# Kernel optimization log

Measured on AMD Instinct MI355X. Metric: run time of the kernel, lower is better.

The kernel has to match this reference:

```python
import jax, jax.numpy as jnp
import numpy as np
from jax import lax

IN_CH, OUT_CH, K = 64, 64, 3
FAN_IN = 8           # LogicNets-style fan-in per output channel (over C_in*K taps)
IN_SCALE, IN_BITS = 0.0625, 8
OUT_SCALE, OUT_BITS = 0.125, 8


def make_mask(seed=7):
    # Binary mask [OUT_CH, IN_CH, K] with exactly FAN_IN ones per output channel
    rng = np.random.RandomState(seed)
    m = np.zeros((OUT_CH, IN_CH * K), dtype=np.float32)
    for o in range(OUT_CH):
        idx = rng.choice(IN_CH * K, size=FAN_IN, replace=False)
        m[o, idx] = 1.0
    return jnp.asarray(m.reshape(OUT_CH, IN_CH, K))


def fake_quant(v, scale, bits):
    # symmetric fake quantization with straight-through estimator
    qmin = -(2 ** (bits - 1))
    qmax = 2 ** (bits - 1) - 1
    q = jnp.clip(jnp.round(v / scale), qmin, qmax) * scale
    return v + lax.stop_gradient(q - v)


def setup_inputs() -> dict:
    key = jax.random.key(0)
    k1, k2 = jax.random.split(key)
    x = jax.random.normal(k1, (512, IN_CH, 1024), dtype=jnp.float32)
    weight = jax.random.normal(k2, (OUT_CH, IN_CH, K), dtype=jnp.float32) * 0.1
    mask = make_mask()
    return {"x": x, "weight": weight, "mask": mask}


def reference(x, weight, mask):
    # input quant
    xq = fake_quant(x, IN_SCALE, IN_BITS)
    # masked (sparse) conv1d, padding=1 (same length)
    w = weight * mask
    out = lax.conv_general_dilated(
        xq, w,
        window_strides=(1,),
        padding=[(1, 1)],
        dimension_numbers=("NCH", "OIH", "NCH"),
    )
    # output quant
    return fake_quant(out, OUT_SCALE, OUT_BITS)
```

## Files before the change

### kernel.cpp

```cpp
#include <hip/hip_runtime.h>

namespace {
constexpr int kInCh  = 64;
constexpr int kOutCh = 64;
constexpr int kK     = 3;
constexpr int kFanIn = 8;
constexpr int kH     = 1024;
constexpr int kTile  = 128;
constexpr int kRow   = kTile + 8;
constexpr int kBlk   = 512;
}

struct Tap { int off; float w; };

__device__ __forceinline__ float quant_in(float v) {
    float q = rintf(v * 16.0f);
    q = fmaxf(q, -128.0f);
    q = fminf(q, 127.0f);
    return q * 0.0625f;
}

__device__ __forceinline__ float quant_out(float v) {
    float q = rintf(v * 8.0f);
    q = fmaxf(q, -128.0f);
    q = fminf(q, 127.0f);
    return q * 0.125f;
}

__global__ void prep_taps(const float* __restrict__ weight,
                          const float* __restrict__ mask,
                          Tap* __restrict__ taps) {
    __shared__ unsigned long long bal[3];
    const int o    = blockIdx.x;
    const int j    = threadIdx.x;
    const int k    = j >> 6;
    const int ci   = j & 63;
    const int idx  = (o * kInCh + ci) * kK + k;

    const float m = mask[idx];
    const unsigned long long b = __ballot(m != 0.0f);
    if (ci == 0) bal[k] = b;
    __syncthreads();

    const unsigned long long lower = b & ((1ull << ci) - 1ull);
    int rank = __popcll(lower);
    #pragma unroll
    for (int w = 0; w < kK; ++w) if (w < k) rank += __popcll(bal[w]);

    if (m != 0.0f && rank < kFanIn) {
        taps[o * kFanIn + rank].off = ci * kRow + k + 3;
        taps[o * kFanIn + rank].w   = weight[idx] * m;
    }
    int total = __popcll(bal[0]) + __popcll(bal[1]) + __popcll(bal[2]);
    if (j >= total && j < kFanIn) {
        taps[o * kFanIn + j].off = 3;
        taps[o * kFanIn + j].w   = 0.0f;
    }
}

__global__ __launch_bounds__(kBlk, 8) void sparse_conv(
        const float* __restrict__ x,
        const Tap*   __restrict__ taps,
        float*       __restrict__ out) {
    __shared__ float sm[kInCh * kRow];

    const int t  = threadIdx.x;
    const int h0 = blockIdx.x * kTile;
    const int n  = blockIdx.y;
    const float* __restrict__ xn = x + (size_t)n * kInCh * kH;

    #pragma unroll
    for (int it = 0; it < 4; ++it) {
        int f  = it * kBlk + t;
        int ci = f >> 5;
        int c4 = f & 31;
        float4 v = reinterpret_cast<const float4*>(xn + ci * kH + h0)[c4];
        v.x = quant_in(v.x); v.y = quant_in(v.y);
        v.z = quant_in(v.z); v.w = quant_in(v.w);
        reinterpret_cast<float4*>(&sm[ci * kRow + 4])[c4] = v;
    }
    if (t < 64) {
        int ci = t;
        float4 v = make_float4(0.f, 0.f, 0.f, 0.f);
        if (h0 > 0) v = *reinterpret_cast<const float4*>(xn + ci * kH + h0 - 4);
        v.x = quant_in(v.x); v.y = quant_in(v.y);
        v.z = quant_in(v.z); v.w = quant_in(v.w);
        *reinterpret_cast<float4*>(&sm[ci * kRow]) = v;
    } else if (t < 128) {
        int ci = t - 64;
        float4 v = make_float4(0.f, 0.f, 0.f, 0.f);
        if (h0 + kTile < kH) v = *reinterpret_cast<const float4*>(xn + ci * kH + h0 + kTile);
        v.x = quant_in(v.x); v.y = quant_in(v.y);
        v.z = quant_in(v.z); v.w = quant_in(v.w);
        *reinterpret_cast<float4*>(&sm[ci * kRow + 4 + kTile]) = v;
    }
    __syncthreads();

    const int g = __builtin_amdgcn_readfirstlane(t >> 6);
    const int i = t & 63;
    float* __restrict__ outn = out + (size_t)n * kOutCh * kH + h0;

    #pragma unroll 2
    for (int oo = 0; oo < 8; ++oo) {
        int o = g * 8 + oo;
        const Tap* __restrict__ tp = taps + o * kFanIn;

        float acc0 = 0.f, acc1 = 0.f;
        #pragma unroll
        for (int j = 0; j < kFanIn; ++j) {
            int off = tp[j].off; float w = tp[j].w;
            acc0 = fmaf(w, sm[off + i],      acc0);
            acc1 = fmaf(w, sm[off + i + 64], acc1);
        }
        outn[o * kH + i]      = quant_out(acc0);
        outn[o * kH + i + 64] = quant_out(acc1);
    }
}

extern "C" void kernel_launch(void* const* d_in, const int* in_sizes, int n_in,
                              void* d_out, int out_size, void* d_ws, size_t ws_size,
                              hipStream_t stream) {
    const float* x      = (const float*)d_in[0];
    const float* weight = (const float*)d_in[1];
    const float* mask   = (const float*)d_in[2];
    float* out = (float*)d_out;
    Tap* taps = (Tap*)d_ws;

    const int nBatch = in_sizes[0] / (kInCh * kH);

    prep_taps<<<kOutCh, kInCh * kK, 0, stream>>>(weight, mask, taps);
    dim3 grid(kH / kTile, nBatch);
    sparse_conv<<<grid, kBlk, 0, stream>>>(x, taps, out);
}
```

Before: 237.6 us.

## Process four tiles per block with register prefetch of next tile

Each block now handles four consecutive 128-wide tiles instead of one, prefetching the next tile's input into registers while computing the current tile, then quantizing and storing into LDS between barriers. This is meant to overlap global loads with compute and amortize block launch overhead. It cuts the grid to a quarter of the blocks and raises register pressure, which may reduce occupancy under the 8-blocks launch bound.

Measured after the change: 250.8 us. +5.6%, slower.

```diff
diff --git a/kernel.cpp b/kernel.cpp
--- a/kernel.cpp
+++ b/kernel.cpp
@@ -9,6 +9,8 @@
 constexpr int kTile  = 128;
 constexpr int kRow   = kTile + 8;
 constexpr int kBlk   = 512;
+constexpr int kTilesPerBlk = 4;
+constexpr int kHTiles = kH / kTile;
 }
 
 struct Tap { int off; float w; };
@@ -64,56 +66,96 @@
         float*       __restrict__ out) {
     __shared__ float sm[kInCh * kRow];
 
-    const int t  = threadIdx.x;
-    const int h0 = blockIdx.x * kTile;
-    const int n  = blockIdx.y;
-    const float* __restrict__ xn = x + (size_t)n * kInCh * kH;
+    const int t = threadIdx.x;
+    const int tau0 = blockIdx.x * kTilesPerBlk;
 
-    #pragma unroll
-    for (int it = 0; it < 4; ++it) {
-        int f  = it * kBlk + t;
-        int ci = f >> 5;
-        int c4 = f & 31;
-        float4 v = reinterpret_cast<const float4*>(xn + ci * kH + h0)[c4];
-        v.x = quant_in(v.x); v.y = quant_in(v.y);
-        v.z = quant_in(v.z); v.w = quant_in(v.w);
-        reinterpret_cast<float4*>(&sm[ci * kRow + 4])[c4] = v;
-    }
-    if (t < 64) {
-        int ci = t;
-        float4 v = make_float4(0.f, 0.f, 0.f, 0.f);
-        if (h0 > 0) v = *reinterpret_cast<const float4*>(xn + ci * kH + h0 - 4);
-        v.x = quant_in(v.x); v.y = quant_in(v.y);
-        v.z = quant_in(v.z); v.w = quant_in(v.w);
-        *reinterpret_cast<float4*>(&sm[ci * kRow]) = v;
-    } else if (t < 128) {
-        int ci = t - 64;
-        float4 v = make_float4(0.f, 0.f, 0.f, 0.f);
-        if (h0 + kTile < kH) v = *reinterpret_cast<const float4*>(xn + ci * kH + h0 + kTile);
-        v.x = quant_in(v.x); v.y = quant_in(v.y);
-        v.z = quant_in(v.z); v.w = quant_in(v.w);
-        *reinterpret_cast<float4*>(&sm[ci * kRow + 4 + kTile]) = v;
-    }
+    float4 r0, r1, r2, r3, rh;
+
+    auto load_regs = [&](int tau) {
+        const int n  = tau >> 3;
+        const int h0 = (tau & 7) * kTile;
+        const float* __restrict__ xn = x + (size_t)n * kInCh * kH;
+        {
+            int f = t;              r0 = reinterpret_cast<const float4*>(xn + (f >> 5) * kH + h0)[f & 31];
+        }
+        {
+            int f = kBlk + t;       r1 = reinterpret_cast<const float4*>(xn + (f >> 5) * kH + h0)[f & 31];
+        }
+        {
+            int f = 2 * kBlk + t;   r2 = reinterpret_cast<const float4*>(xn + (f >> 5) * kH + h0)[f & 31];
+        }
+        {
+            int f = 3 * kBlk + t;   r3 = reinterpret_cast<const float4*>(xn + (f >> 5) * kH + h0)[f & 31];
+        }
+        rh = make_float4(0.f, 0.f, 0.f, 0.f);
+        if (t < 64) {
+            if (h0 > 0) rh = *reinterpret_cast<const float4*>(xn + t * kH + h0 - 4);
+        } else if (t < 128) {
+            if (h0 + kTile < kH) rh = *reinterpret_cast<const float4*>(xn + (t - 64) * kH + h0 + kTile);
+        }
+    };
+
+    auto store_lds = [&](void) {
+        auto q4 = [](float4 v) {
+            v.x = quant_in(v.x); v.y = quant_in(v.y);
+            v.z = quant_in(v.z); v.w = quant_in(v.w);
+            return v;
+        };
+        {
+            int f = t;            reinterpret_cast<float4*>(&sm[(f >> 5) * kRow + 4])[f & 31] = q4(r0);
+        }
+        {
+            int f = kBlk + t;     reinterpret_cast<float4*>(&sm[(f >> 5) * kRow + 4])[f & 31] = q4(r1);
+        }
+        {
+            int f = 2 * kBlk + t; reinterpret_cast<float4*>(&sm[(f >> 5) * kRow + 4])[f & 31] = q4(r2);
+        }
+        {
+            int f = 3 * kBlk + t; reinterpret_cast<float4*>(&sm[(f >> 5) * kRow + 4])[f & 31] = q4(r3);
+        }
+        if (t < 64) {
+            *reinterpret_cast<float4*>(&sm[t * kRow]) = q4(rh);
+        } else if (t < 128) {
+            *reinterpret_cast<float4*>(&sm[(t - 64) * kRow + 4 + kTile]) = q4(rh);
+        }
+    };
+
+    load_regs(tau0);
+    store_lds();
     __syncthreads();
 
     const int g = __builtin_amdgcn_readfirstlane(t >> 6);
     const int i = t & 63;
-    float* __restrict__ outn = out + (size_t)n * kOutCh * kH + h0;
 
-    #pragma unroll 2
-    for (int oo = 0; oo < 8; ++oo) {
-        int o = g * 8 + oo;
-        const Tap* __restrict__ tp = taps + o * kFanIn;
+    #pragma unroll
+    for (int it = 0; it < kTilesPerBlk; ++it) {
+        const int tau = tau0 + it;
+        const int n   = tau >> 3;
+        const int h0  = (tau & 7) * kTile;
 
-        float acc0 = 0.f, acc1 = 0.f;
-        #pragma unroll
-        for (int j = 0; j < kFanIn; ++j) {
-            int off = tp[j].off; float w = tp[j].w;
-            acc0 = fmaf(w, sm[off + i],      acc0);
-            acc1 = fmaf(w, sm[off + i + 64], acc1);
+        if (it + 1 < kTilesPerBlk) load_regs(tau + 1);
+
+        float* __restrict__ outn = out + (size_t)n * kOutCh * kH + h0;
+        #pragma unroll 2
+        for (int oo = 0; oo < 8; ++oo) {
+            int o = g * 8 + oo;
+            const Tap* __restrict__ tp = taps + o * kFanIn;
+            float acc0 = 0.f, acc1 = 0.f;
+            #pragma unroll
+            for (int j = 0; j < kFanIn; ++j) {
+                int off = tp[j].off; float w = tp[j].w;
+                acc0 = fmaf(w, sm[off + i],      acc0);
+                acc1 = fmaf(w, sm[off + i + 64], acc1);
+            }
+            outn[o * kH + i]      = quant_out(acc0);
+            outn[o * kH + i + 64] = quant_out(acc1);
         }
-        outn[o * kH + i]      = quant_out(acc0);
-        outn[o * kH + i + 64] = quant_out(acc1);
+
+        if (it + 1 < kTilesPerBlk) {
+            __syncthreads();
+            store_lds();
+            __syncthreads();
+        }
     }
 }
 
@@ -127,8 +169,9 @@
     Tap* taps = (Tap*)d_ws;
 
     const int nBatch = in_sizes[0] / (kInCh * kH);
+    const int nTiles = nBatch * kHTiles;
+    const int nBlocks = nTiles / kTilesPerBlk;
 
     prep_taps<<<kOutCh, kInCh * kK, 0, stream>>>(weight, mask, taps);
-    dim3 grid(kH / kTile, nBatch);
-    sparse_conv<<<grid, kBlk, 0, stream>>>(x, taps, out);
+    sparse_conv<<<nBlocks, kBlk, 0, stream>>>(x, taps, out);
 }
```
